# Optimization experiments

Hardware: AMD Instinct MI355X
Metric: run time of the kernel (lower is better)

## Reference

```python
import jax, jax.numpy as jnp
import numpy as np

B = 64          # graphs per batch
N = 131072      # total nodes (B * 2048)
E = 524288      # total edges
V = 32000       # embedding vocab
D_IN = 256      # embed.output_size
D = 128         # GCN hidden size


def setup_inputs() -> dict:
    key = jax.random.key(0)
    ks = jax.random.split(key, 9)
    return {
        "node_tokens": jax.random.randint(ks[0], (N,), 0, V),
        "edge_index": jax.random.randint(ks[1], (2, E), 0, N),
        "embed_table": jax.random.normal(ks[2], (V, D_IN), jnp.float32),
        "W_node_w": jax.random.normal(ks[3], (D, D_IN), jnp.float32) * 0.02,
        "W_node_b": jax.random.normal(ks[4], (D,), jnp.float32) * 0.02,
        "conv1_w": jax.random.normal(ks[5], (D, D), jnp.float32) * 0.02,
        "conv1_b": jax.random.normal(ks[6], (D,), jnp.float32) * 0.02,
        "conv2_w": jax.random.normal(ks[7], (D, D), jnp.float32) * 0.02,
        "conv2_b": jax.random.normal(ks[8], (D,), jnp.float32) * 0.02,
    }


def _gcn_conv(x, src, dst, norm, W, b):
    # PyG GCNConv: linear first, then normalized scatter-add aggregation, then bias.
    x = x @ W.T                                        # [N, D]
    msg = x[src] * norm[:, None]                       # gather + per-edge scale
    out = jax.ops.segment_sum(msg, dst, num_segments=N)  # scatter-add at dst
    return out + b


def reference(node_tokens, edge_index, embed_table, W_node_w, W_node_b,
              conv1_w, conv1_b, conv2_w, conv2_b):
    # compute_node_features: embed lookup -> W_node linear (no mask path)
    x = embed_table[node_tokens] @ W_node_w.T + W_node_b   # [N, D]

    # GCNConv normalization with self-loops (shared by both layers)
    loop = jnp.arange(N)
    src = jnp.concatenate([edge_index[0], loop])
    dst = jnp.concatenate([edge_index[1], loop])
    deg = jax.ops.segment_sum(jnp.ones(E + N, x.dtype), dst, num_segments=N)
    dinv = jnp.where(deg > 0, jax.lax.rsqrt(deg), 0.0)
    norm = dinv[src] * dinv[dst]                           # [E+N]

    x = jax.nn.relu(_gcn_conv(x, src, dst, norm, conv1_w, conv1_b))
    x = _gcn_conv(x, src, dst, norm, conv2_w, conv2_b)

    # Unpad into [B, max_n, D]; equal-length graphs, no edge tokens -> reshape.
    n = N // B
    output = x.reshape(B, n, D)          # dropout_p=0 -> identity
    labels = node_tokens.reshape(B, n)
    labels_mask = jnp.ones((B, n), dtype=bool)
    label_node_ids = jnp.broadcast_to(jnp.arange(n), (B, n))
    return output, labels, labels_mask, label_node_ids
```

## Files before the change

kernel.cpp:

```cpp
#include <hip/hip_runtime.h>
#include <hip/hip_bf16.h>

#define N_NODES 131072
#define N_EDGES 524288
#define DHID    128
#define DIN     256

typedef __attribute__((ext_vector_type(8))) short short8;
typedef __attribute__((ext_vector_type(4))) float floatx4;

__device__ inline short bf16_rne(float f) {
    union { float f; unsigned u; } v; v.f = f;
    unsigned r = v.u + 0x7FFF + ((v.u >> 16) & 1);
    return (short)(r >> 16);
}
__device__ inline float bf16_to_f(short s) {
    union { unsigned u; float f; } v; v.u = ((unsigned)(unsigned short)s) << 16;
    return v.f;
}


__global__ __launch_bounds__(256) void mega_prep(const float* __restrict__ emb,
                                                 short* __restrict__ embb,
                                                 const float* __restrict__ Wn,
                                                 const float* __restrict__ W1,
                                                 const float* __restrict__ W2,
                                                 short* __restrict__ Wnb,
                                                 short* __restrict__ W1b,
                                                 short* __restrict__ W2b,
                                                 const int* __restrict__ edst,
                                                 int* __restrict__ counts) {
    const int b = blockIdx.x;
    if (b < 4000) {
        size_t i = (size_t)(b * 256 + threadIdx.x) * 8;
        float4 v0 = *(const float4*)&emb[i];
        float4 v1 = *(const float4*)&emb[i + 4];
        short8 o;
        o[0] = bf16_rne(v0.x); o[1] = bf16_rne(v0.y);
        o[2] = bf16_rne(v0.z); o[3] = bf16_rne(v0.w);
        o[4] = bf16_rne(v1.x); o[5] = bf16_rne(v1.y);
        o[6] = bf16_rne(v1.z); o[7] = bf16_rne(v1.w);
        *(short8*)&embb[i] = o;
    } else if (b < 4256) {
        int i = (b - 4000) * 256 + threadIdx.x;
        if (i < 32768)      Wnb[i] = bf16_rne(Wn[i]);
        else if (i < 49152) W1b[i - 32768] = bf16_rne(W1[i - 32768]);
        else                W2b[i - 49152] = bf16_rne(W2[i - 49152]);
    } else {
        int e = (b - 4256) * 256 + threadIdx.x;
        atomicAdd(&counts[edst[e]], 1);
    }
}


__global__ __launch_bounds__(256) void alloc_csr(const int* __restrict__ counts,
                                                 int* __restrict__ offsets,
                                                 int* __restrict__ cursor,
                                                 float* __restrict__ dinv,
                                                 int* __restrict__ total) {
    __shared__ int s[256];
    __shared__ int base;
    int i = blockIdx.x * 256 + threadIdx.x;
    int v = counts[i];
    s[threadIdx.x] = v;
    __syncthreads();
    for (int d = 1; d < 256; d <<= 1) {
        int t = (threadIdx.x >= d) ? s[threadIdx.x - d] : 0;
        __syncthreads();
        s[threadIdx.x] += t;
        __syncthreads();
    }
    int incl = s[threadIdx.x];
    if (threadIdx.x == 255) base = atomicAdd(total, incl);
    __syncthreads();
    int off = base + incl - v;
    offsets[i] = off;
    cursor[i]  = off;
    dinv[i] = rsqrtf((float)(v + 1));
}

__global__ __launch_bounds__(256) void fill_csr(const int* __restrict__ src,
                                                const int* __restrict__ dst,
                                                int* __restrict__ cursor,
                                                const float* __restrict__ dinv,
                                                int2* __restrict__ csr) {
    int e = blockIdx.x * 256 + threadIdx.x;
    int d = dst[e];
    int s = src[e];
    int p = atomicAdd(&cursor[d], 1);
    csr[p] = make_int2(s, __float_as_int(dinv[s]));
}


__global__ __launch_bounds__(256) void gemm_embed(const short* __restrict__ Ab,
                                                  const int* __restrict__ tok,
                                                  const short* __restrict__ Wb,
                                                  const float* __restrict__ bias,
                                                  short* __restrict__ out,
                                                  float* __restrict__ meta_out) {
    const int t = threadIdx.x;
    const int wid  = t >> 6;
    const int lane = t & 63;
    const int col  = lane & 15;
    const int quad = lane >> 4;
    const int base = blockIdx.x * 128 + wid * 32;

    if (t < 128) {
        int i = blockIdx.x * 128 + t;
        const size_t L0 = (size_t)N_NODES * DHID;
        meta_out[L0 + i]               = (float)tok[i];
        meta_out[L0 + N_NODES + i]     = 1.0f;
        meta_out[L0 + 2 * N_NODES + i] = (float)(i & 2047);
    }

    const size_t row0 = (size_t)tok[base + col];
    const size_t row1 = (size_t)tok[base + 16 + col];

    floatx4 acc[2][8] = {};

#pragma unroll
    for (int kc = 0; kc < DIN / 32; ++kc) {
        const int ko = kc * 32 + quad * 8;
        short8 a0 = *(const short8*)&Ab[row0 * DIN + ko];
        short8 a1 = *(const short8*)&Ab[row1 * DIN + ko];
#pragma unroll
        for (int ft = 0; ft < 8; ++ft) {
            short8 b = *(const short8*)&Wb[(size_t)(col * 8 + ft) * DIN + ko];
            acc[0][ft] = __builtin_amdgcn_mfma_f32_16x16x32_bf16(a0, b, acc[0][ft], 0, 0, 0);
            acc[1][ft] = __builtin_amdgcn_mfma_f32_16x16x32_bf16(a1, b, acc[1][ft], 0, 0, 0);
        }
    }

    const float4 bv0 = *(const float4*)&bias[col * 8];
    const float4 bv1 = *(const float4*)&bias[col * 8 + 4];
    const float bb[8] = {bv0.x, bv0.y, bv0.z, bv0.w, bv1.x, bv1.y, bv1.z, bv1.w};

#pragma unroll
    for (int mt = 0; mt < 2; ++mt) {
#pragma unroll
        for (int r = 0; r < 4; ++r) {
            const int row = base + mt * 16 + quad * 4 + r;
            short8 o;
#pragma unroll
            for (int ft = 0; ft < 8; ++ft)
                o[ft] = bf16_rne(acc[mt][ft][r] + bb[ft]);
            *(short8*)&out[(size_t)row * DHID + col * 8] = o;
        }
    }
}


template <bool RELU, bool OUT_BF16>
__global__ __launch_bounds__(256, 8) void fused_conv(const short* __restrict__ x,
                                                     const int2* __restrict__ csr,
                                                     const int* __restrict__ offsets,
                                                     const int* __restrict__ counts,
                                                     const float* __restrict__ dinv,
                                                     const short* __restrict__ Wb,
                                                     const float* __restrict__ bias,
                                                     void* __restrict__ outp) {
    const int t = threadIdx.x;
    const int wid  = t >> 6;
    const int lane = t & 63;
    const int col  = lane & 15;
    const int quad = lane >> 4;
    const int base = (blockIdx.x * 4 + wid) * 16;
    const int node = base + col;

    const float di = dinv[node];
    const int beg = offsets[node];
    const int cnt = counts[node];
    const int2* pcsr = csr + beg;

    float af[4][8];
    {
        const size_t xrow = (size_t)node * DHID + quad * 8;
#pragma unroll
        for (int c = 0; c < 4; ++c) {
            short8 v = *(const short8*)&x[xrow + c * 32];
#pragma unroll
            for (int j = 0; j < 8; ++j) af[c][j] = di * bf16_to_f(v[j]);
        }
    }

    int2 cn = (cnt > 0) ? pcsr[0] : make_int2(0, 0);
    for (int e = 0; e < cnt; ++e) {
        const int   s = cn.x;
        const float w = __int_as_float(cn.y);
        if (e + 1 < cnt) cn = pcsr[e + 1];
        const size_t r0 = (size_t)s * DHID + quad * 8;
        short8 u0 = *(const short8*)&x[r0];
        short8 u1 = *(const short8*)&x[r0 + 32];
        short8 u2 = *(const short8*)&x[r0 + 64];
        short8 u3 = *(const short8*)&x[r0 + 96];
#pragma unroll
        for (int j = 0; j < 8; ++j) {
            af[0][j] = fmaf(w, bf16_to_f(u0[j]), af[0][j]);
            af[1][j] = fmaf(w, bf16_to_f(u1[j]), af[1][j]);
            af[2][j] = fmaf(w, bf16_to_f(u2[j]), af[2][j]);
            af[3][j] = fmaf(w, bf16_to_f(u3[j]), af[3][j]);
        }
    }

    short8 a[4];
#pragma unroll
    for (int c = 0; c < 4; ++c)
#pragma unroll
        for (int j = 0; j < 8; ++j) a[c][j] = bf16_rne(di * af[c][j]);

    floatx4 acc[8] = {};
#pragma unroll
    for (int c = 0; c < 4; ++c) {
        const int ko = c * 32 + quad * 8;
#pragma unroll
        for (int ft = 0; ft < 8; ++ft) {
            short8 b = *(const short8*)&Wb[(size_t)(col * 8 + ft) * DHID + ko];
            acc[ft] = __builtin_amdgcn_mfma_f32_16x16x32_bf16(a[c], b, acc[ft], 0, 0, 0);
        }
    }

    const float4 bv0 = *(const float4*)&bias[col * 8];
    const float4 bv1 = *(const float4*)&bias[col * 8 + 4];
    const float bb[8] = {bv0.x, bv0.y, bv0.z, bv0.w, bv1.x, bv1.y, bv1.z, bv1.w};
    short* outb = (short*)outp;
    float* outf = (float*)outp;
#pragma unroll
    for (int r = 0; r < 4; ++r) {
        const size_t row = (size_t)(base + quad * 4 + r) * DHID + col * 8;
        if (OUT_BF16) {
            short8 o;
#pragma unroll
            for (int ft = 0; ft < 8; ++ft) {
                float v = acc[ft][r] + bb[ft];
                if (RELU) v = fmaxf(v, 0.f);
                o[ft] = bf16_rne(v);
            }
            *(short8*)&outb[row] = o;
        } else {
            float4 o0, o1;
            o0.x = acc[0][r] + bb[0]; o0.y = acc[1][r] + bb[1];
            o0.z = acc[2][r] + bb[2]; o0.w = acc[3][r] + bb[3];
            o1.x = acc[4][r] + bb[4]; o1.y = acc[5][r] + bb[5];
            o1.z = acc[6][r] + bb[6]; o1.w = acc[7][r] + bb[7];
            if (RELU) {
                o0.x = fmaxf(o0.x, 0.f); o0.y = fmaxf(o0.y, 0.f);
                o0.z = fmaxf(o0.z, 0.f); o0.w = fmaxf(o0.w, 0.f);
                o1.x = fmaxf(o1.x, 0.f); o1.y = fmaxf(o1.y, 0.f);
                o1.z = fmaxf(o1.z, 0.f); o1.w = fmaxf(o1.w, 0.f);
            }
            *(float4*)&outf[row] = o0;
            *(float4*)&outf[row + 4] = o1;
        }
    }
}


extern "C" void kernel_launch(void* const* d_in, const int* in_sizes, int n_in,
                              void* d_out, int out_size, void* d_ws, size_t ws_size,
                              hipStream_t stream) {
    const int*   tok  = (const int*)d_in[0];
    const int*   esrc = (const int*)d_in[1];
    const int*   edst = esrc + N_EDGES;
    const float* emb  = (const float*)d_in[2];
    const float* Wn   = (const float*)d_in[3];
    const float* bn   = (const float*)d_in[4];
    const float* W1   = (const float*)d_in[5];
    const float* b1   = (const float*)d_in[6];
    const float* W2   = (const float*)d_in[7];
    const float* b2   = (const float*)d_in[8];
    float* out = (float*)d_out;

    char* ws = (char*)d_ws;
    int*   counts  = (int*)(ws);
    int*   total   = (int*)(ws + (1u << 19));
    int*   offsets = (int*)(ws + (1u << 19) + 256);
    int*   cursor  = (int*)(ws + (2u << 19) + 256);
    float* dinv    = (float*)(ws + (3u << 19) + 256);
    int2*  csr     = (int2*)(ws + 3 * (1u << 20));
    short* Wnb     = (short*)(ws + 7 * (1u << 20));
    short* W1b     = (short*)(ws + 7 * (1u << 20) + (1u << 16));
    short* W2b     = (short*)(ws + 7 * (1u << 20) + 96 * 1024);
    short* embb    = (short*)(ws + 7 * (1u << 20) + (1u << 18));
    short* x2b     = (short*)(ws + 24 * (1u << 20));
    short* xb      = (short*)d_out;

    hipMemsetAsync(counts, 0, (1u << 19) + 256, stream);
    mega_prep<<<4256 + N_EDGES / 256, 256, 0, stream>>>(
        emb, embb, Wn, W1, W2, Wnb, W1b, W2b, edst, counts);
    alloc_csr<<<N_NODES / 256, 256, 0, stream>>>(counts, offsets, cursor, dinv, total);
    fill_csr<<<N_EDGES / 256, 256, 0, stream>>>(esrc, edst, cursor, dinv, csr);

    gemm_embed<<<N_NODES / 128, 256, 0, stream>>>(embb, tok, Wnb, bn, xb, out);
    fused_conv<true, true><<<N_NODES / 64, 256, 0, stream>>>(
        xb, csr, offsets, counts, dinv, W1b, b1, x2b);
    fused_conv<false, false><<<N_NODES / 64, 256, 0, stream>>>(
        x2b, csr, offsets, counts, dinv, W2b, b2, out);
}
```

Before: 336.9 us.

## Precompute vocab-level embedding projection and gather it directly in first conv

Instead of converting the whole embedding table to bf16 and running a per-node GEMM, the projection is computed once per vocabulary row (32000 rows, fewer than the 131072 nodes) into a table z. The first GCN layer then gathers z rows through token ids stored in an int4 CSR entry and adds the bias scaled by the summed edge weights. This removes the full-table bf16 conversion pass and the separate embed GEMM kernel, and the metadata writes move into alloc_csr. In exchange the CSR entries double in size, the first conv does an extra token indirection, and bf16 rounding now happens at a different point.

```diff
diff --git a/kernel.cpp b/kernel.cpp
--- a/kernel.cpp
+++ b/kernel.cpp
@@ -5,6 +5,7 @@
 #define N_EDGES 524288
 #define DHID    128
 #define DIN     256
+#define VOCAB   32000
 
 typedef __attribute__((ext_vector_type(8))) short short8;
 typedef __attribute__((ext_vector_type(4))) float floatx4;
@@ -18,36 +19,75 @@
     union { unsigned u; float f; } v; v.u = ((unsigned)(unsigned short)s) << 16;
     return v.f;
 }
-
-
-__global__ __launch_bounds__(256) void mega_prep(const float* __restrict__ emb,
-                                                 short* __restrict__ embb,
-                                                 const float* __restrict__ Wn,
-                                                 const float* __restrict__ W1,
-                                                 const float* __restrict__ W2,
-                                                 short* __restrict__ Wnb,
-                                                 short* __restrict__ W1b,
-                                                 short* __restrict__ W2b,
-                                                 const int* __restrict__ edst,
-                                                 int* __restrict__ counts) {
+__device__ inline short8 cvt8(float4 lo, float4 hi) {
+    short8 o;
+    o[0] = bf16_rne(lo.x); o[1] = bf16_rne(lo.y);
+    o[2] = bf16_rne(lo.z); o[3] = bf16_rne(lo.w);
+    o[4] = bf16_rne(hi.x); o[5] = bf16_rne(hi.y);
+    o[6] = bf16_rne(hi.z); o[7] = bf16_rne(hi.w);
+    return o;
+}
+
+
+#define MEGA_VB 250
+#define MEGA_WB 128
+#define MEGA_TOTAL (MEGA_VB + MEGA_WB + N_EDGES / 256)
+
+__global__ __launch_bounds__(256) void mega(const float* __restrict__ emb,
+                                            const float* __restrict__ Wn,
+                                            short* __restrict__ z,
+                                            const float* __restrict__ W1,
+                                            const float* __restrict__ W2,
+                                            short* __restrict__ W1b,
+                                            short* __restrict__ W2b,
+                                            const int* __restrict__ edst,
+                                            int* __restrict__ counts) {
     const int b = blockIdx.x;
-    if (b < 4000) {
-        size_t i = (size_t)(b * 256 + threadIdx.x) * 8;
-        float4 v0 = *(const float4*)&emb[i];
-        float4 v1 = *(const float4*)&emb[i + 4];
-        short8 o;
-        o[0] = bf16_rne(v0.x); o[1] = bf16_rne(v0.y);
-        o[2] = bf16_rne(v0.z); o[3] = bf16_rne(v0.w);
-        o[4] = bf16_rne(v1.x); o[5] = bf16_rne(v1.y);
-        o[6] = bf16_rne(v1.z); o[7] = bf16_rne(v1.w);
-        *(short8*)&embb[i] = o;
-    } else if (b < 4256) {
-        int i = (b - 4000) * 256 + threadIdx.x;
-        if (i < 32768)      Wnb[i] = bf16_rne(Wn[i]);
-        else if (i < 49152) W1b[i - 32768] = bf16_rne(W1[i - 32768]);
-        else                W2b[i - 49152] = bf16_rne(W2[i - 49152]);
+    if (b < MEGA_VB) {
+        const int t = threadIdx.x;
+        const int wid  = t >> 6;
+        const int lane = t & 63;
+        const int col  = lane & 15;
+        const int quad = lane >> 4;
+        const int vbase = b * 128 + wid * 32;
+        const size_t row0 = (size_t)(vbase + col);
+        const size_t row1 = (size_t)(vbase + 16 + col);
+
+        floatx4 acc[2][8] = {};
+#pragma unroll
+        for (int kc = 0; kc < DIN / 32; ++kc) {
+            const int ko = kc * 32 + quad * 8;
+            short8 a0 = cvt8(*(const float4*)&emb[row0 * DIN + ko],
+                             *(const float4*)&emb[row0 * DIN + ko + 4]);
+            short8 a1 = cvt8(*(const float4*)&emb[row1 * DIN + ko],
+                             *(const float4*)&emb[row1 * DIN + ko + 4]);
+#pragma unroll
+            for (int ft = 0; ft < 8; ++ft) {
+                const size_t wr = (size_t)(col * 8 + ft) * DIN + ko;
+                short8 bb = cvt8(*(const float4*)&Wn[wr],
+                                 *(const float4*)&Wn[wr + 4]);
+                acc[0][ft] = __builtin_amdgcn_mfma_f32_16x16x32_bf16(a0, bb, acc[0][ft], 0, 0, 0);
+                acc[1][ft] = __builtin_amdgcn_mfma_f32_16x16x32_bf16(a1, bb, acc[1][ft], 0, 0, 0);
+            }
+        }
+#pragma unroll
+        for (int mt = 0; mt < 2; ++mt) {
+#pragma unroll
+            for (int r = 0; r < 4; ++r) {
+                const int row = vbase + mt * 16 + quad * 4 + r;
+                short8 o;
+#pragma unroll
+                for (int ft = 0; ft < 8; ++ft)
+                    o[ft] = bf16_rne(acc[mt][ft][r]);
+                *(short8*)&z[(size_t)row * DHID + col * 8] = o;
+            }
+        }
+    } else if (b < MEGA_VB + MEGA_WB) {
+        int i = (b - MEGA_VB) * 256 + threadIdx.x;
+        if (i < 16384) W1b[i] = bf16_rne(W1[i]);
+        else           W2b[i - 16384] = bf16_rne(W2[i - 16384]);
     } else {
-        int e = (b - 4256) * 256 + threadIdx.x;
+        int e = (b - MEGA_VB - MEGA_WB) * 256 + threadIdx.x;
         atomicAdd(&counts[edst[e]], 1);
     }
 }
@@ -57,7 +97,9 @@
                                                  int* __restrict__ offsets,
                                                  int* __restrict__ cursor,
                                                  float* __restrict__ dinv,
-                                                 int* __restrict__ total) {
+                                                 int* __restrict__ total,
+                                                 const int* __restrict__ tok,
+                                                 float* __restrict__ meta_out) {
     __shared__ int s[256];
     __shared__ int base;
     int i = blockIdx.x * 256 + threadIdx.x;
@@ -77,85 +119,35 @@
     offsets[i] = off;
     cursor[i]  = off;
     dinv[i] = rsqrtf((float)(v + 1));
+
+    const size_t L0 = (size_t)N_NODES * DHID;
+    meta_out[L0 + i]               = (float)tok[i];
+    meta_out[L0 + N_NODES + i]     = 1.0f;
+    meta_out[L0 + 2 * N_NODES + i] = (float)(i & 2047);
 }
 
 __global__ __launch_bounds__(256) void fill_csr(const int* __restrict__ src,
                                                 const int* __restrict__ dst,
                                                 int* __restrict__ cursor,
                                                 const float* __restrict__ dinv,
-                                                int2* __restrict__ csr) {
+                                                const int* __restrict__ tok,
+                                                int4* __restrict__ csr) {
     int e = blockIdx.x * 256 + threadIdx.x;
     int d = dst[e];
     int s = src[e];
     int p = atomicAdd(&cursor[d], 1);
-    csr[p] = make_int2(s, __float_as_int(dinv[s]));
-}
-
-
-__global__ __launch_bounds__(256) void gemm_embed(const short* __restrict__ Ab,
-                                                  const int* __restrict__ tok,
-                                                  const short* __restrict__ Wb,
-                                                  const float* __restrict__ bias,
-                                                  short* __restrict__ out,
-                                                  float* __restrict__ meta_out) {
-    const int t = threadIdx.x;
-    const int wid  = t >> 6;
-    const int lane = t & 63;
-    const int col  = lane & 15;
-    const int quad = lane >> 4;
-    const int base = blockIdx.x * 128 + wid * 32;
-
-    if (t < 128) {
-        int i = blockIdx.x * 128 + t;
-        const size_t L0 = (size_t)N_NODES * DHID;
-        meta_out[L0 + i]               = (float)tok[i];
-        meta_out[L0 + N_NODES + i]     = 1.0f;
-        meta_out[L0 + 2 * N_NODES + i] = (float)(i & 2047);
-    }
-
-    const size_t row0 = (size_t)tok[base + col];
-    const size_t row1 = (size_t)tok[base + 16 + col];
-
-    floatx4 acc[2][8] = {};
-
-#pragma unroll
-    for (int kc = 0; kc < DIN / 32; ++kc) {
-        const int ko = kc * 32 + quad * 8;
-        short8 a0 = *(const short8*)&Ab[row0 * DIN + ko];
-        short8 a1 = *(const short8*)&Ab[row1 * DIN + ko];
-#pragma unroll
-        for (int ft = 0; ft < 8; ++ft) {
-            short8 b = *(const short8*)&Wb[(size_t)(col * 8 + ft) * DIN + ko];
-            acc[0][ft] = __builtin_amdgcn_mfma_f32_16x16x32_bf16(a0, b, acc[0][ft], 0, 0, 0);
-            acc[1][ft] = __builtin_amdgcn_mfma_f32_16x16x32_bf16(a1, b, acc[1][ft], 0, 0, 0);
-        }
-    }
-
-    const float4 bv0 = *(const float4*)&bias[col * 8];
-    const float4 bv1 = *(const float4*)&bias[col * 8 + 4];
-    const float bb[8] = {bv0.x, bv0.y, bv0.z, bv0.w, bv1.x, bv1.y, bv1.z, bv1.w};
-
-#pragma unroll
-    for (int mt = 0; mt < 2; ++mt) {
-#pragma unroll
-        for (int r = 0; r < 4; ++r) {
-            const int row = base + mt * 16 + quad * 4 + r;
-            short8 o;
-#pragma unroll
-            for (int ft = 0; ft < 8; ++ft)
-                o[ft] = bf16_rne(acc[mt][ft][r] + bb[ft]);
-            *(short8*)&out[(size_t)row * DHID + col * 8] = o;
-        }
-    }
-}
-
-
-template <bool RELU, bool OUT_BF16>
+    csr[p] = make_int4(s, tok[s], __float_as_int(dinv[s]), 0);
+}
+
+
+template <bool RELU, bool OUT_BF16, bool ZG>
 __global__ __launch_bounds__(256, 8) void fused_conv(const short* __restrict__ x,
-                                                     const int2* __restrict__ csr,
+                                                     const int4* __restrict__ csr,
                                                      const int* __restrict__ offsets,
                                                      const int* __restrict__ counts,
                                                      const float* __restrict__ dinv,
+                                                     const int* __restrict__ tok,
+                                                     const float* __restrict__ bn,
                                                      const short* __restrict__ Wb,
                                                      const float* __restrict__ bias,
                                                      void* __restrict__ outp) {
@@ -170,11 +162,12 @@
     const float di = dinv[node];
     const int beg = offsets[node];
     const int cnt = counts[node];
-    const int2* pcsr = csr + beg;
+    const int4* pcsr = csr + beg;
 
     float af[4][8];
     {
-        const size_t xrow = (size_t)node * DHID + quad * 8;
+        const int self = ZG ? tok[node] : node;
+        const size_t xrow = (size_t)self * DHID + quad * 8;
 #pragma unroll
         for (int c = 0; c < 4; ++c) {
             short8 v = *(const short8*)&x[xrow + c * 32];
@@ -182,12 +175,14 @@
             for (int j = 0; j < 8; ++j) af[c][j] = di * bf16_to_f(v[j]);
         }
     }
-
-    int2 cn = (cnt > 0) ? pcsr[0] : make_int2(0, 0);
+    float sw = di;
+
+    int4 cn = (cnt > 0) ? pcsr[0] : make_int4(0, 0, 0, 0);
     for (int e = 0; e < cnt; ++e) {
-        const int   s = cn.x;
-        const float w = __int_as_float(cn.y);
+        const int   s = ZG ? cn.y : cn.x;
+        const float w = __int_as_float(cn.z);
         if (e + 1 < cnt) cn = pcsr[e + 1];
+        if (ZG) sw += w;
         const size_t r0 = (size_t)s * DHID + quad * 8;
         short8 u0 = *(const short8*)&x[r0];
         short8 u1 = *(const short8*)&x[r0 + 32];
@@ -204,9 +199,19 @@
 
     short8 a[4];
 #pragma unroll
-    for (int c = 0; c < 4; ++c)
-#pragma unroll
-        for (int j = 0; j < 8; ++j) a[c][j] = bf16_rne(di * af[c][j]);
+    for (int c = 0; c < 4; ++c) {
+        if (ZG) {
+            const float4 b0 = *(const float4*)&bn[c * 32 + quad * 8];
+            const float4 b1 = *(const float4*)&bn[c * 32 + quad * 8 + 4];
+            const float bv[8] = {b0.x, b0.y, b0.z, b0.w, b1.x, b1.y, b1.z, b1.w};
+#pragma unroll
+            for (int j = 0; j < 8; ++j)
+                a[c][j] = bf16_rne(di * (af[c][j] + sw * bv[j]));
+        } else {
+#pragma unroll
+            for (int j = 0; j < 8; ++j) a[c][j] = bf16_rne(di * af[c][j]);
+        }
+    }
 
     floatx4 acc[8] = {};
 #pragma unroll
@@ -276,23 +281,20 @@
     int*   offsets = (int*)(ws + (1u << 19) + 256);
     int*   cursor  = (int*)(ws + (2u << 19) + 256);
     float* dinv    = (float*)(ws + (3u << 19) + 256);
-    int2*  csr     = (int2*)(ws + 3 * (1u << 20));
-    short* Wnb     = (short*)(ws + 7 * (1u << 20));
-    short* W1b     = (short*)(ws + 7 * (1u << 20) + (1u << 16));
-    short* W2b     = (short*)(ws + 7 * (1u << 20) + 96 * 1024);
-    short* embb    = (short*)(ws + 7 * (1u << 20) + (1u << 18));
+    int4*  csr     = (int4*)(ws + 3 * (1u << 20));
+    short* W1b     = (short*)(ws + 11 * (1u << 20));
+    short* W2b     = (short*)(ws + 11 * (1u << 20) + (1u << 15));
+    short* z       = (short*)(ws + 12 * (1u << 20));
     short* x2b     = (short*)(ws + 24 * (1u << 20));
-    short* xb      = (short*)d_out;
 
     hipMemsetAsync(counts, 0, (1u << 19) + 256, stream);
-    mega_prep<<<4256 + N_EDGES / 256, 256, 0, stream>>>(
-        emb, embb, Wn, W1, W2, Wnb, W1b, W2b, edst, counts);
-    alloc_csr<<<N_NODES / 256, 256, 0, stream>>>(counts, offsets, cursor, dinv, total);
-    fill_csr<<<N_EDGES / 256, 256, 0, stream>>>(esrc, edst, cursor, dinv, csr);
-
-    gemm_embed<<<N_NODES / 128, 256, 0, stream>>>(embb, tok, Wnb, bn, xb, out);
-    fused_conv<true, true><<<N_NODES / 64, 256, 0, stream>>>(
-        xb, csr, offsets, counts, dinv, W1b, b1, x2b);
-    fused_conv<false, false><<<N_NODES / 64, 256, 0, stream>>>(
-        x2b, csr, offsets, counts, dinv, W2b, b2, out);
-}
+    mega<<<MEGA_TOTAL, 256, 0, stream>>>(emb, Wn, z, W1, W2, W1b, W2b, edst, counts);
+    alloc_csr<<<N_NODES / 256, 256, 0, stream>>>(counts, offsets, cursor, dinv,
+                                                 total, tok, out);
+    fill_csr<<<N_EDGES / 256, 256, 0, stream>>>(esrc, edst, cursor, dinv, tok, csr);
+
+    fused_conv<true, true, true><<<N_NODES / 64, 256, 0, stream>>>(
+        z, csr, offsets, counts, dinv, tok, bn, W1b, b1, x2b);
+    fused_conv<false, false, false><<<N_NODES / 64, 256, 0, stream>>>(
+        x2b, csr, offsets, counts, dinv, tok, bn, W2b, b2, out);
+}
```

After: 286.8 us. -14.9%, faster.
